# Kernel tuning notes

Measured on AMD Instinct MI355X. Metric: run time of the kernel, lower is better.

The kernel has to match this reference:

```python
import jax, jax.numpy as jnp
import numpy as np

VOCAB, EMBED, HIDDEN, NCLS = 50257, 1024, 4096, 3
B, S = 4096, 128


def ternary_quant(w):
    # Per-tensor ternary quantization: scale = mean |w|, weights in {-s, 0, +s}.
    s = jnp.mean(jnp.abs(w))
    return jnp.round(jnp.clip(w / s, -1.0, 1.0)) * s


def layer_norm(x, g, b, eps=1e-5):
    mu = jnp.mean(x, axis=-1, keepdims=True)
    var = jnp.mean(jnp.square(x - mu), axis=-1, keepdims=True)
    return (x - mu) * jax.lax.rsqrt(var + eps) * g + b


def setup_inputs() -> dict:
    key = jax.random.key(0)
    ks = jax.random.split(key, 12)
    input_ids = jax.random.randint(ks[0], (B, S), 0, VOCAB, dtype=jnp.int32)
    emb = jax.random.normal(ks[1], (VOCAB, EMBED), dtype=jnp.float32) * 0.02
    emb = emb.at[0].set(0.0)  # padding_idx=0
    w1 = jax.random.normal(ks[2], (HIDDEN, EMBED), dtype=jnp.float32) * 0.02
    b1 = jnp.zeros((HIDDEN,), jnp.float32)
    w2 = jax.random.normal(ks[3], (HIDDEN // 2, HIDDEN), dtype=jnp.float32) * 0.02
    b2 = jnp.zeros((HIDDEN // 2,), jnp.float32)
    w3 = jax.random.normal(ks[4], (NCLS, HIDDEN // 2), dtype=jnp.float32) * 0.02
    b3 = jnp.zeros((NCLS,), jnp.float32)
    g1 = jnp.ones((HIDDEN,), jnp.float32)
    beta1 = jnp.zeros((HIDDEN,), jnp.float32)
    g2 = jnp.ones((HIDDEN // 2,), jnp.float32)
    beta2 = jnp.zeros((HIDDEN // 2,), jnp.float32)
    return dict(input_ids=input_ids, emb=emb, w1=w1, b1=b1, w2=w2, b2=b2,
                w3=w3, b3=b3, g1=g1, beta1=beta1, g2=g2, beta2=beta2)


def reference(input_ids, emb, w1, b1, w2, b2, w3, b3, g1, beta1, g2, beta2):
    x = emb[input_ids]                                   # (B, S, E)
    mask = (input_ids != 0).astype(x.dtype)[..., None]   # (B, S, 1)
    x = jnp.sum(x * mask, axis=1) / jnp.clip(jnp.sum(mask, axis=1), 1.0)  # (B, E)
    h = jax.nn.gelu(layer_norm(x @ ternary_quant(w1).T + b1, g1, beta1), approximate=False)
    h = jax.nn.gelu(layer_norm(h @ ternary_quant(w2).T + b2, g2, beta2), approximate=False)
    logits = h @ ternary_quant(w3).T + b3                # (B, 3)
    return logits
```

## Files before the change

kernel.cpp:

```cpp
#include <hip/hip_runtime.h>
#include <cstdint>
#include <cstddef>


#define GAS __attribute__((address_space(1)))
#define LAS __attribute__((address_space(3)))

typedef __bf16 bf16x8 __attribute__((ext_vector_type(8)));
typedef float  f32x4  __attribute__((ext_vector_type(4)));
typedef unsigned short u16x8 __attribute__((ext_vector_type(8)));

__device__ __forceinline__ unsigned short f2bf(float f) {
    unsigned int u = __float_as_uint(f);
    u += 0x7FFFu + ((u >> 16) & 1u);
    return (unsigned short)(u >> 16);
}
__device__ __forceinline__ float bf2f(unsigned short h) {
    return __uint_as_float(((unsigned int)h) << 16);
}

static constexpr int BB = 4096;
static constexpr int SS = 128;
static constexpr int EE = 1024;
static constexpr int HH = 4096;
static constexpr int H2D = 2048;
static constexpr int VOCAB = 50257;

static constexpr size_t MiB      = 1024 * 1024;
static constexpr size_t OFF_S    = 0;
static constexpr size_t OFF_X    = 65536;
static constexpr size_t OFF_EMBH = OFF_X + (size_t)BB * EE * 2;
static constexpr size_t SZ_EMBH  = (size_t)VOCAB * EE * 2;
static constexpr size_t OFF_Q1   = OFF_EMBH;
static constexpr size_t OFF_Q2   = OFF_EMBH + 8 * MiB;
static constexpr size_t OFF_C1   = OFF_EMBH + 24 * MiB;
static constexpr size_t OFF_C2   = OFF_EMBH + 24 * MiB;
static constexpr size_t OFF_H2   = OFF_EMBH;
static constexpr size_t OFF_H1   = OFF_EMBH + SZ_EMBH;


__global__ __launch_bounds__(256) void prep2_kernel(const float* __restrict__ e,
                                                    unsigned short* __restrict__ o,
                                                    const float* __restrict__ w1,
                                                    const float* __restrict__ w2,
                                                    double* __restrict__ part1,
                                                    double* __restrict__ part2) {
    const int bid = blockIdx.x;
    const int tid = threadIdx.x;
    const int n8 = (VOCAB * EE) / 8;
    for (int i = bid * 256 + tid; i < n8; i += 2048 * 256) {
        const float4 v0 = ((const float4*)e)[2 * i];
        const float4 v1 = ((const float4*)e)[2 * i + 1];
        union { unsigned short u[8]; uint4 q; } r;
        r.u[0] = f2bf(v0.x); r.u[1] = f2bf(v0.y); r.u[2] = f2bf(v0.z); r.u[3] = f2bf(v0.w);
        r.u[4] = f2bf(v1.x); r.u[5] = f2bf(v1.y); r.u[6] = f2bf(v1.z); r.u[7] = f2bf(v1.w);
        ((uint4*)o)[i] = r.q;
    }
    const int lane = tid & 63, wid = tid >> 6;
    double a1 = 0.0, a2 = 0.0;
    const int n41 = HH * EE / 4;
    for (int i = bid * 256 + tid; i < n41; i += 2048 * 256) {
        const float4 v = ((const float4*)w1)[i];
        a1 += (double)fabsf(v.x) + (double)fabsf(v.y) + (double)fabsf(v.z) + (double)fabsf(v.w);
    }
    const int n42 = H2D * HH / 4;
    for (int i = bid * 256 + tid; i < n42; i += 2048 * 256) {
        const float4 v = ((const float4*)w2)[i];
        a2 += (double)fabsf(v.x) + (double)fabsf(v.y) + (double)fabsf(v.z) + (double)fabsf(v.w);
    }
    for (int off = 32; off; off >>= 1) { a1 += __shfl_down(a1, off); a2 += __shfl_down(a2, off); }
    __shared__ double r1[4], r2[4];
    if (lane == 0) { r1[wid] = a1; r2[wid] = a2; }
    __syncthreads();
    if (tid == 0) {
        part1[bid] = r1[0] + r1[1] + r1[2] + r1[3];
        part2[bid] = r2[0] + r2[1] + r2[2] + r2[3];
    }
}

__global__ __launch_bounds__(256) void reduce_sums(const double* __restrict__ part1,
                                                   const double* __restrict__ part2,
                                                   const float* __restrict__ w3,
                                                   double* __restrict__ sums) {
    const int bid = blockIdx.x, tid = threadIdx.x;
    const int lane = tid & 63, wid = tid >> 6;
    double acc = 0.0;
    if (bid == 0) {
        for (int i = tid; i < 2048; i += 256) acc += part1[i];
    } else if (bid == 1) {
        for (int i = tid; i < 2048; i += 256) acc += part2[i];
    } else {
        for (int i = tid; i < 3 * H2D; i += 256) acc += (double)fabsf(w3[i]);
    }
    for (int o = 32; o; o >>= 1) acc += __shfl_down(acc, o);
    __shared__ double r[4];
    if (lane == 0) r[wid] = acc;
    __syncthreads();
    if (tid == 0) sums[bid] = r[0] + r[1] + r[2] + r[3];
}

__global__ __launch_bounds__(256) void quant_all(const float* __restrict__ w1,
                                                 const float* __restrict__ w2,
                                                 const double* __restrict__ sums,
                                                 unsigned short* __restrict__ q1,
                                                 unsigned short* __restrict__ q2) {
    const int bid = blockIdx.x;
    const float* w; int n8; unsigned short* q; int b0; int nb; double ssum; double dn;
    if (bid < 2048) { w = w1; n8 = HH * EE / 8;  q = q1; b0 = bid;        nb = 2048; ssum = sums[0]; dn = (double)HH * EE;  }
    else            { w = w2; n8 = H2D * HH / 8; q = q2; b0 = bid - 2048; nb = 4096; ssum = sums[1]; dn = (double)H2D * HH; }
    const float inv_s = (float)(dn / ssum);
    for (int i = b0 * 256 + threadIdx.x; i < n8; i += nb * 256) {
        const float4 v0 = ((const float4*)w)[2 * i];
        const float4 v1 = ((const float4*)w)[2 * i + 1];
        union { unsigned short u[8]; uint4 p; } r;
        const float a[8] = {v0.x, v0.y, v0.z, v0.w, v1.x, v1.y, v1.z, v1.w};
        #pragma unroll
        for (int j = 0; j < 8; ++j)
            r.u[j] = f2bf(rintf(fminf(1.f, fmaxf(-1.f, a[j] * inv_s))));
        ((uint4*)q)[i] = r.p;
    }
}

__global__ __launch_bounds__(256) void pool_kernel(const int* __restrict__ ids,
                                                   const unsigned short* __restrict__ embh,
                                                   unsigned short* __restrict__ X) {
    const int tid = threadIdx.x;
    const int row = tid >> 7;
    const int t   = tid & 127;
    __shared__ int sid[256];
    __shared__ int sorted_ids[2][128];
    __shared__ int cnt[2][64];
    __shared__ int pos[2][64];
    __shared__ int nz[2];
    sid[tid] = ids[(size_t)blockIdx.x * 256 + tid];
    if (tid < 128) ((int*)cnt)[tid] = 0;
    if (tid < 2) nz[tid] = 0;
    __syncthreads();
    const int myid = sid[tid];
    const int ph = myid >> 10;
    atomicAdd(&cnt[row][ph], 1);
    if (myid != 0) atomicAdd(&nz[row], 1);
    __syncthreads();
    if (tid < 2) {
        int s = 0;
        #pragma unroll
        for (int p = 0; p < 64; ++p) { pos[tid][p] = s; s += cnt[tid][p]; }
    }
    __syncthreads();
    const int where = atomicAdd(&pos[row][ph], 1);
    sorted_ids[row][where] = myid;
    __syncthreads();

    const int col = t * 8;
    float a[8] = {};
    #pragma unroll 8
    for (int s = 0; s < 128; ++s) {
        const int id = sorted_ids[row][s];
        const u16x8 v = *(const u16x8*)(embh + (size_t)id * EE + col);
        #pragma unroll
        for (int j = 0; j < 8; ++j) a[j] += bf2f(v[j]);
    }
    const int c = nz[row];
    const float inv = 1.f / (float)(c ? c : 1);
    u16x8 ov;
    #pragma unroll
    for (int j = 0; j < 8; ++j) ov[j] = f2bf(a[j] * inv);
    const int b = blockIdx.x * 2 + row;
    *(u16x8*)(X + (size_t)b * EE + col) = ov;
}


#define FENCE_ asm volatile("" ::: "memory")
#define SBAR_  do { FENCE_; __builtin_amdgcn_s_barrier(); FENCE_; } while (0)
#define WAITLGKM_ do { asm volatile("s_waitcnt lgkmcnt(0)" ::: "memory"); __builtin_amdgcn_sched_barrier(0); } while (0)

#define LDA_(dst, b, i, ks) dst = *(const LAS bf16x8*)((LAS char*)lds + (b) * 32768 + aBase0 + (ks) * 8192 + (i) * 1024)
#define LDB_(dst, b, j, ks) dst = *(const LAS bf16x8*)((LAS char*)lds + (b) * 32768 + bBase0 + (ks) * 8192 + (j) * 1024)

#define STAGE_(gptr, rowBase, t_, slotOff)                                                         \
    {                                                                                              \
        const unsigned short* g0_ = (gptr) + (size_t)((rowBase) + srow) * K + kStart + (t_) * 64 + scol; \
        __builtin_amdgcn_global_load_lds((const GAS void*)g0_,                                     \
            (LAS void*)((LAS char*)lds + (slotOff) + wid * 1024), 16, 0, 0);                       \
        __builtin_amdgcn_global_load_lds((const GAS void*)(g0_ + 32),                              \
            (LAS void*)((LAS char*)lds + (slotOff) + 8192 + wid * 1024), 16, 0, 0);                \
    }

#define MFMA16_(ib, bfA, jb)                                                                       \
    _Pragma("unroll") for (int ii = 0; ii < 4; ++ii) {                                             \
        _Pragma("unroll") for (int jj = 0; jj < 2; ++jj) {                                         \
            f32x4 c_ = acc[(ib) * 4 + ii][(jb) + jj];                                              \
            c_ = __builtin_amdgcn_mfma_f32_16x16x32_bf16(af[ii][0], bfA[jj][0], c_, 0, 0, 0);      \
            c_ = __builtin_amdgcn_mfma_f32_16x16x32_bf16(af[ii][1], bfA[jj][1], c_, 0, 0, 0);      \
            acc[(ib) * 4 + ii][(jb) + jj] = c_;                                                    \
        }                                                                                          \
    }

#define GROUP_(b, t_)                                                                              \
    {                                                                                              \
        _Pragma("unroll") for (int ii = 0; ii < 4; ++ii) { LDA_(af[ii][0], b, ii, 0); LDA_(af[ii][1], b, ii, 1); } \
        _Pragma("unroll") for (int jj = 0; jj < 2; ++jj) { LDB_(bf0[jj][0], b, jj, 0); LDB_(bf0[jj][1], b, jj, 1); } \
        if ((t_) + 1 < NTI) {                                                                      \
            STAGE_(A, mBase, (t_) + 1, ((b) ^ 1) * 32768);                                         \
            STAGE_(A, mBase + 128, (t_) + 1, ((b) ^ 1) * 32768 + 16384);                           \
        }                                                                                          \
        SBAR_; WAITLGKM_;                                                                          \
        __builtin_amdgcn_s_setprio(1); MFMA16_(0, bf0, 0); __builtin_amdgcn_s_setprio(0);          \
        SBAR_;                                                                                     \
        _Pragma("unroll") for (int jj = 0; jj < 2; ++jj) { LDB_(bf1[jj][0], b, 2 + jj, 0); LDB_(bf1[jj][1], b, 2 + jj, 1); } \
        if ((t_) + 1 < NTI) { STAGE_(B, nBase + 128, (t_) + 1, 65536 + ((b) ^ 1) * 32768 + 16384); } \
        SBAR_; WAITLGKM_;                                                                          \
        __builtin_amdgcn_s_setprio(1); MFMA16_(0, bf1, 2); __builtin_amdgcn_s_setprio(0);          \
        SBAR_;                                                                                     \
        _Pragma("unroll") for (int ii = 0; ii < 4; ++ii) { LDA_(af[ii][0], b, 4 + ii, 0); LDA_(af[ii][1], b, 4 + ii, 1); } \
        if ((t_) + 2 < NTI) { STAGE_(B, nBase, (t_) + 2, 65536 + (b) * 32768); }                   \
        SBAR_; WAITLGKM_;                                                                          \
        __builtin_amdgcn_s_setprio(1); MFMA16_(1, bf0, 0); __builtin_amdgcn_s_setprio(0);          \
        SBAR_;                                                                                     \
        __builtin_amdgcn_s_setprio(1); MFMA16_(1, bf1, 2); __builtin_amdgcn_s_setprio(0);          \
        if ((t_) + 2 < NTI) { asm volatile("s_waitcnt vmcnt(2)" ::: "memory"); }                   \
        else               { asm volatile("s_waitcnt vmcnt(0)" ::: "memory"); }                    \
        SBAR_;                                                                                     \
    }

#define GEMM256_CORE(NT_VAL)                                                                       \
    extern __shared__ char lds[];                                                                  \
    constexpr int NTI = (NT_VAL);                                                                  \
    const int tid  = threadIdx.x;                                                                  \
    const int wid  = tid >> 6;                                                                     \
    const int lane = tid & 63;                                                                     \
    const int wm = wid >> 2, wn = wid & 3;                                                         \
    const int quad = lane >> 4;                                                                    \
    const int l16  = lane & 15;                                                                    \
    const int mBase = blockIdx.y * 256;                                                            \
    const int nBase = blockIdx.x * 256;                                                            \
    const int kStart = blockIdx.z * NTI * 64;                                                      \
                    \
                    \
    const int dp   = wid * 1024 + lane * 16;                                                       \
    const int srow = dp >> 6;                                                                      \
    const int sb   = dp & 63;                                                                      \
    const int scol = ((((sb >> 5) & 1) ^ ((srow >> 3) & 1)) << 4) + (((sb >> 4) & 1) << 3);        \
                           \
    const int qoff = ((quad ^ (((l16 >> 3) & 1) << 1)) << 4);                                      \
    const int aBase0 = (wm << 14) + (l16 << 6) + qoff;                                             \
    const int bBase0 = 65536 + ((wn >> 1) << 14) + ((((wn & 1) << 6) + l16) << 6) + qoff;          \
    f32x4 acc[8][4] = {};                                                                          \
    bf16x8 af[4][2], bf0[2][2], bf1[2][2];                                                         \
              \
    STAGE_(A, mBase, 0, 0);                                                                        \
    STAGE_(A, mBase + 128, 0, 16384);                                                              \
    STAGE_(B, nBase, 0, 65536);                                                                    \
    STAGE_(B, nBase + 128, 0, 65536 + 16384);                                                      \
    STAGE_(B, nBase, 1, 65536 + 32768);                                                            \
    asm volatile("s_waitcnt vmcnt(2)" ::: "memory");                                               \
    SBAR_;                                                                                         \
    _Pragma("unroll 1")                                                                            \
    for (int t = 0; t < NTI; t += 2) {                                                             \
        GROUP_(0, t)                                                                               \
        GROUP_(1, t + 1)                                                                           \
    }

__global__ __launch_bounds__(512, 2) void gemm256_c16(const unsigned short* __restrict__ A,
                                                      const unsigned short* __restrict__ B,
                                                      unsigned short* __restrict__ C,
                                                      int M, int N, int K) {
    GEMM256_CORE(16)
    #pragma unroll
    for (int i = 0; i < 8; ++i) {
        const int row0 = mBase + wm * 128 + i * 16 + quad * 4;
        #pragma unroll
        for (int j = 0; j < 4; ++j) {
            const int col = nBase + wn * 64 + j * 16 + l16;
            #pragma unroll
            for (int r = 0; r < 4; ++r)
                C[(size_t)(row0 + r) * N + col] = f2bf(acc[i][j][r]);
        }
    }
}

__global__ __launch_bounds__(512, 2) void gemm256_sk2(const unsigned short* __restrict__ A,
                                                      const unsigned short* __restrict__ B,
                                                      float* __restrict__ Cp,
                                                      int M, int N, int K) {
    GEMM256_CORE(32)
    float* C = Cp + (size_t)blockIdx.z * M * N;
    #pragma unroll
    for (int i = 0; i < 8; ++i) {
        const int row0 = mBase + wm * 128 + i * 16 + quad * 4;
        #pragma unroll
        for (int j = 0; j < 4; ++j) {
            const int col = nBase + wn * 64 + j * 16 + l16;
            #pragma unroll
            for (int r = 0; r < 4; ++r)
                C[(size_t)(row0 + r) * N + col] = acc[i][j][r];
        }
    }
}

__global__ __launch_bounds__(256) void ln_gelu_c16(const unsigned short* __restrict__ Cm,
                                                   const double* __restrict__ ssum, double nw,
                                                   const float* __restrict__ bias,
                                                   const float* __restrict__ gamma,
                                                   const float* __restrict__ beta,
                                                   unsigned short* __restrict__ H, int N) {
    __shared__ float buf[4096];
    __shared__ float redS[4], redQ[4];
    const int row = blockIdx.x, tid = threadIdx.x;
    const int lane = tid & 63, wid = tid >> 6;
    const float s = (float)(ssum[0] / nw);
    float ps = 0.f, pq = 0.f;
    for (int c = tid; c < N; c += 256) {
        const float y = bf2f(Cm[(size_t)row * N + c]) * s + bias[c];
        buf[c] = y;
        ps += y; pq += y * y;
    }
    for (int o = 32; o; o >>= 1) { ps += __shfl_down(ps, o); pq += __shfl_down(pq, o); }
    if (lane == 0) { redS[wid] = ps; redQ[wid] = pq; }
    __syncthreads();
    const float sum = redS[0] + redS[1] + redS[2] + redS[3];
    const float sq  = redQ[0] + redQ[1] + redQ[2] + redQ[3];
    const float mu  = sum / (float)N;
    float var = sq / (float)N - mu * mu;
    var = fmaxf(var, 0.f);
    const float inv = rsqrtf(var + 1e-5f);
    for (int c = tid; c < N; c += 256) {
        const float y = (buf[c] - mu) * inv * gamma[c] + beta[c];
        const float g = 0.5f * y * (1.f + erff(y * 0.70710678118654752f));
        H[(size_t)row * N + c] = f2bf(g);
    }
}

__global__ __launch_bounds__(256) void ln_gelu_2buf(const float* __restrict__ Ca,
                                                    const float* __restrict__ Cb,
                                                    const double* __restrict__ ssum, double nw,
                                                    const float* __restrict__ bias,
                                                    const float* __restrict__ gamma,
                                                    const float* __restrict__ beta,
                                                    unsigned short* __restrict__ H, int N) {
    __shared__ float buf[2048];
    __shared__ float redS[4], redQ[4];
    const int row = blockIdx.x, tid = threadIdx.x;
    const int lane = tid & 63, wid = tid >> 6;
    const float s = (float)(ssum[0] / nw);
    float ps = 0.f, pq = 0.f;
    for (int c = tid; c < N; c += 256) {
        const size_t idx = (size_t)row * N + c;
        const float y = (Ca[idx] + Cb[idx]) * s + bias[c];
        buf[c] = y;
        ps += y; pq += y * y;
    }
    for (int o = 32; o; o >>= 1) { ps += __shfl_down(ps, o); pq += __shfl_down(pq, o); }
    if (lane == 0) { redS[wid] = ps; redQ[wid] = pq; }
    __syncthreads();
    const float sum = redS[0] + redS[1] + redS[2] + redS[3];
    const float sq  = redQ[0] + redQ[1] + redQ[2] + redQ[3];
    const float mu  = sum / (float)N;
    float var = sq / (float)N - mu * mu;
    var = fmaxf(var, 0.f);
    const float inv = rsqrtf(var + 1e-5f);
    for (int c = tid; c < N; c += 256) {
        const float y = (buf[c] - mu) * inv * gamma[c] + beta[c];
        const float g = 0.5f * y * (1.f + erff(y * 0.70710678118654752f));
        H[(size_t)row * N + c] = f2bf(g);
    }
}

__global__ __launch_bounds__(256) void final_kernel(const unsigned short* __restrict__ H2,
                                                    const float* __restrict__ w3,
                                                    const double* __restrict__ ssum,
                                                    const float* __restrict__ b3,
                                                    float* __restrict__ out) {
    const int row = blockIdx.x, tid = threadIdx.x;
    const int lane = tid & 63, wid = tid >> 6;
    const float inv_s3 = (float)((double)(3 * H2D) / ssum[0]);
    float a0 = 0.f, a1 = 0.f, a2 = 0.f;
    for (int k = tid; k < H2D; k += 256) {
        const float h = bf2f(H2[(size_t)row * H2D + k]);
        const float q0 = rintf(fminf(1.f, fmaxf(-1.f, w3[k] * inv_s3)));
        const float q1 = rintf(fminf(1.f, fmaxf(-1.f, w3[H2D + k] * inv_s3)));
        const float q2 = rintf(fminf(1.f, fmaxf(-1.f, w3[2 * H2D + k] * inv_s3)));
        a0 += h * q0; a1 += h * q1; a2 += h * q2;
    }
    for (int o = 32; o; o >>= 1) {
        a0 += __shfl_down(a0, o); a1 += __shfl_down(a1, o); a2 += __shfl_down(a2, o);
    }
    __shared__ float r[3][4];
    if (lane == 0) { r[0][wid] = a0; r[1][wid] = a1; r[2][wid] = a2; }
    __syncthreads();
    if (tid < 3) {
        const float s3 = (float)(ssum[0] / (double)(3 * H2D));
        out[(size_t)row * 3 + tid] =
            (r[tid][0] + r[tid][1] + r[tid][2] + r[tid][3]) * s3 + b3[tid];
    }
}


extern "C" void kernel_launch(void* const* d_in, const int* in_sizes, int n_in,
                              void* d_out, int out_size, void* d_ws, size_t ws_size,
                              hipStream_t stream) {
    const int*   ids = (const int*)d_in[0];
    const float* emb = (const float*)d_in[1];
    const float* w1  = (const float*)d_in[2];
    const float* b1  = (const float*)d_in[3];
    const float* w2  = (const float*)d_in[4];
    const float* b2  = (const float*)d_in[5];
    const float* w3  = (const float*)d_in[6];
    const float* b3  = (const float*)d_in[7];
    const float* g1  = (const float*)d_in[8];
    const float* be1 = (const float*)d_in[9];
    const float* g2  = (const float*)d_in[10];
    const float* be2 = (const float*)d_in[11];
    float* out = (float*)d_out;
    char* ws = (char*)d_ws;

    double*         sums  = (double*)(ws + OFF_S);
    double*         part1 = sums + 8;
    double*         part2 = part1 + 2048;
    unsigned short* X     = (unsigned short*)(ws + OFF_X);
    unsigned short* embh  = (unsigned short*)(ws + OFF_EMBH);
    unsigned short* q1    = (unsigned short*)(ws + OFF_Q1);
    unsigned short* q2    = (unsigned short*)(ws + OFF_Q2);
    unsigned short* C1    = (unsigned short*)(ws + OFF_C1);
    float*          Cp    = (float*)(ws + OFF_C2);
    unsigned short* H1    = (unsigned short*)(ws + OFF_H1);
    unsigned short* H2    = (unsigned short*)(ws + OFF_H2);

    static int gemmAttrDone = 0;
    if (!gemmAttrDone) {
        hipFuncSetAttribute((const void*)gemm256_c16,
                            hipFuncAttributeMaxDynamicSharedMemorySize, 131072);
        hipFuncSetAttribute((const void*)gemm256_sk2,
                            hipFuncAttributeMaxDynamicSharedMemorySize, 131072);
        gemmAttrDone = 1;
    }

    prep2_kernel<<<2048, 256, 0, stream>>>(emb, embh, w1, w2, part1, part2);
    reduce_sums<<<3, 256, 0, stream>>>(part1, part2, w3, sums);
    pool_kernel<<<BB / 2, 256, 0, stream>>>(ids, embh, X);

    quant_all<<<6144, 256, 0, stream>>>(w1, w2, sums, q1, q2);

    gemm256_c16<<<dim3(HH / 256, BB / 256), 512, 131072, stream>>>(X, q1, C1, BB, HH, EE);
    ln_gelu_c16<<<BB, 256, 0, stream>>>(C1, sums + 0, (double)HH * (double)EE,
                                        b1, g1, be1, H1, HH);
    gemm256_sk2<<<dim3(H2D / 256, BB / 256, 2), 512, 131072, stream>>>(H1, q2, Cp, BB, H2D, HH);
    ln_gelu_2buf<<<BB, 256, 0, stream>>>(Cp, Cp + (size_t)BB * H2D, sums + 1,
                                         (double)H2D * (double)HH, b2, g2, be2, H2, H2D);
    final_kernel<<<BB, 256, 0, stream>>>(H2, w3, sums + 2, b3, out);
}
```

Before: 659.1 us.

## Fuse quantization into pooling, LN2+GELU into final classifier, register-resident layer norm

Merges the weight ternary quantization into the pooling kernel, so each pool block also quantizes a slice of w1 and w2. The q1/q2 buffers move to offsets past H1 so they no longer alias the bf16 embedding copy that pooling reads. The second layer-norm+GELU is fused with the 3-class projection, removing the H2 round trip and one launch. Both layer norms now keep values in registers with vectorized loads instead of a shared-memory buffer. This cuts launches and intermediate traffic but adds register pressure and longer pool blocks.

```diff
diff --git a/kernel.cpp b/kernel.cpp
--- a/kernel.cpp
+++ b/kernel.cpp
@@ -31,12 +31,11 @@
 static constexpr size_t OFF_X    = 65536;
 static constexpr size_t OFF_EMBH = OFF_X + (size_t)BB * EE * 2;
 static constexpr size_t SZ_EMBH  = (size_t)VOCAB * EE * 2;
-static constexpr size_t OFF_Q1   = OFF_EMBH;
-static constexpr size_t OFF_Q2   = OFF_EMBH + 8 * MiB;
 static constexpr size_t OFF_C1   = OFF_EMBH + 24 * MiB;
 static constexpr size_t OFF_C2   = OFF_EMBH + 24 * MiB;
-static constexpr size_t OFF_H2   = OFF_EMBH;
 static constexpr size_t OFF_H1   = OFF_EMBH + SZ_EMBH;
+static constexpr size_t OFF_Q1   = OFF_H1 + 32 * MiB;
+static constexpr size_t OFF_Q2   = OFF_Q1 + 8 * MiB;
 
 
 __global__ __launch_bounds__(256) void prep2_kernel(const float* __restrict__ e,
@@ -99,32 +98,17 @@
     if (tid == 0) sums[bid] = r[0] + r[1] + r[2] + r[3];
 }
 
-__global__ __launch_bounds__(256) void quant_all(const float* __restrict__ w1,
-                                                 const float* __restrict__ w2,
-                                                 const double* __restrict__ sums,
-                                                 unsigned short* __restrict__ q1,
-                                                 unsigned short* __restrict__ q2) {
+__global__ __launch_bounds__(256) void pool_quant(const int* __restrict__ ids,
+                                                  const unsigned short* __restrict__ embh,
+                                                  unsigned short* __restrict__ X,
+                                                  const float* __restrict__ w1,
+                                                  const float* __restrict__ w2,
+                                                  const double* __restrict__ sums,
+                                                  unsigned short* __restrict__ q1,
+                                                  unsigned short* __restrict__ q2) {
+    const int tid = threadIdx.x;
     const int bid = blockIdx.x;
-    const float* w; int n8; unsigned short* q; int b0; int nb; double ssum; double dn;
-    if (bid < 2048) { w = w1; n8 = HH * EE / 8;  q = q1; b0 = bid;        nb = 2048; ssum = sums[0]; dn = (double)HH * EE;  }
-    else            { w = w2; n8 = H2D * HH / 8; q = q2; b0 = bid - 2048; nb = 4096; ssum = sums[1]; dn = (double)H2D * HH; }
-    const float inv_s = (float)(dn / ssum);
-    for (int i = b0 * 256 + threadIdx.x; i < n8; i += nb * 256) {
-        const float4 v0 = ((const float4*)w)[2 * i];
-        const float4 v1 = ((const float4*)w)[2 * i + 1];
-        union { unsigned short u[8]; uint4 p; } r;
-        const float a[8] = {v0.x, v0.y, v0.z, v0.w, v1.x, v1.y, v1.z, v1.w};
-        #pragma unroll
-        for (int j = 0; j < 8; ++j)
-            r.u[j] = f2bf(rintf(fminf(1.f, fmaxf(-1.f, a[j] * inv_s))));
-        ((uint4*)q)[i] = r.p;
-    }
-}
-
-__global__ __launch_bounds__(256) void pool_kernel(const int* __restrict__ ids,
-                                                   const unsigned short* __restrict__ embh,
-                                                   unsigned short* __restrict__ X) {
-    const int tid = threadIdx.x;
+
     const int row = tid >> 7;
     const int t   = tid & 127;
     __shared__ int sid[256];
@@ -132,7 +116,7 @@
     __shared__ int cnt[2][64];
     __shared__ int pos[2][64];
     __shared__ int nz[2];
-    sid[tid] = ids[(size_t)blockIdx.x * 256 + tid];
+    sid[tid] = ids[(size_t)bid * 256 + tid];
     if (tid < 128) ((int*)cnt)[tid] = 0;
     if (tid < 2) nz[tid] = 0;
     __syncthreads();
@@ -150,6 +134,34 @@
     const int where = atomicAdd(&pos[row][ph], 1);
     sorted_ids[row][where] = myid;
     __syncthreads();
+
+    {
+        const int i = bid * 256 + tid;
+        const float inv1 = (float)((double)HH * (double)EE / sums[0]);
+        {
+            const float4 v0 = ((const float4*)w1)[2 * i];
+            const float4 v1 = ((const float4*)w1)[2 * i + 1];
+            union { unsigned short u[8]; uint4 p; } r;
+            const float a[8] = {v0.x, v0.y, v0.z, v0.w, v1.x, v1.y, v1.z, v1.w};
+            #pragma unroll
+            for (int j = 0; j < 8; ++j)
+                r.u[j] = f2bf(rintf(fminf(1.f, fmaxf(-1.f, a[j] * inv1))));
+            ((uint4*)q1)[i] = r.p;
+        }
+        const float inv2 = (float)((double)H2D * (double)HH / sums[1]);
+        #pragma unroll
+        for (int k = 0; k < 2; ++k) {
+            const int j8 = i + k * (2048 * 256);
+            const float4 v0 = ((const float4*)w2)[2 * j8];
+            const float4 v1 = ((const float4*)w2)[2 * j8 + 1];
+            union { unsigned short u[8]; uint4 p; } r;
+            const float a[8] = {v0.x, v0.y, v0.z, v0.w, v1.x, v1.y, v1.z, v1.w};
+            #pragma unroll
+            for (int j = 0; j < 8; ++j)
+                r.u[j] = f2bf(rintf(fminf(1.f, fmaxf(-1.f, a[j] * inv2))));
+            ((uint4*)q2)[j8] = r.p;
+        }
+    }
 
     const int col = t * 8;
     float a[8] = {};
@@ -165,7 +177,7 @@
     u16x8 ov;
     #pragma unroll
     for (int j = 0; j < 8; ++j) ov[j] = f2bf(a[j] * inv);
-    const int b = blockIdx.x * 2 + row;
+    const int b = bid * 2 + row;
     *(u16x8*)(X + (size_t)b * EE + col) = ov;
 }
 
@@ -235,19 +247,15 @@
     const int mBase = blockIdx.y * 256;                                                            \
     const int nBase = blockIdx.x * 256;                                                            \
     const int kStart = blockIdx.z * NTI * 64;                                                      \
-                    \
-                    \
     const int dp   = wid * 1024 + lane * 16;                                                       \
     const int srow = dp >> 6;                                                                      \
     const int sb   = dp & 63;                                                                      \
     const int scol = ((((sb >> 5) & 1) ^ ((srow >> 3) & 1)) << 4) + (((sb >> 4) & 1) << 3);        \
-                           \
     const int qoff = ((quad ^ (((l16 >> 3) & 1) << 1)) << 4);                                      \
     const int aBase0 = (wm << 14) + (l16 << 6) + qoff;                                             \
     const int bBase0 = 65536 + ((wn >> 1) << 14) + ((((wn & 1) << 6) + l16) << 6) + qoff;          \
     f32x4 acc[8][4] = {};                                                                          \
     bf16x8 af[4][2], bf0[2][2], bf1[2][2];                                                         \
-              \
     STAGE_(A, mBase, 0, 0);                                                                        \
     STAGE_(A, mBase + 128, 0, 16384);                                                              \
     STAGE_(B, nBase, 0, 65536);                                                                    \
@@ -304,16 +312,25 @@
                                                    const float* __restrict__ gamma,
                                                    const float* __restrict__ beta,
                                                    unsigned short* __restrict__ H, int N) {
-    __shared__ float buf[4096];
     __shared__ float redS[4], redQ[4];
     const int row = blockIdx.x, tid = threadIdx.x;
     const int lane = tid & 63, wid = tid >> 6;
     const float s = (float)(ssum[0] / nw);
+    float y[16];
     float ps = 0.f, pq = 0.f;
-    for (int c = tid; c < N; c += 256) {
-        const float y = bf2f(Cm[(size_t)row * N + c]) * s + bias[c];
-        buf[c] = y;
-        ps += y; pq += y * y;
+    #pragma unroll
+    for (int h = 0; h < 2; ++h) {
+        const int c = h * 2048 + tid * 8;
+        const u16x8 v = *(const u16x8*)(Cm + (size_t)row * N + c);
+        const float4 b0 = *(const float4*)(bias + c);
+        const float4 b1 = *(const float4*)(bias + c + 4);
+        #pragma unroll
+        for (int j = 0; j < 4; ++j) {
+            const float y0 = bf2f(v[j]) * s + ((const float*)&b0)[j];
+            const float y1 = bf2f(v[4 + j]) * s + ((const float*)&b1)[j];
+            y[h * 8 + j] = y0; y[h * 8 + 4 + j] = y1;
+            ps += y0 + y1; pq += y0 * y0 + y1 * y1;
+        }
     }
     for (int o = 32; o; o >>= 1) { ps += __shfl_down(ps, o); pq += __shfl_down(pq, o); }
     if (lane == 0) { redS[wid] = ps; redQ[wid] = pq; }
@@ -324,74 +341,93 @@
     float var = sq / (float)N - mu * mu;
     var = fmaxf(var, 0.f);
     const float inv = rsqrtf(var + 1e-5f);
-    for (int c = tid; c < N; c += 256) {
-        const float y = (buf[c] - mu) * inv * gamma[c] + beta[c];
-        const float g = 0.5f * y * (1.f + erff(y * 0.70710678118654752f));
-        H[(size_t)row * N + c] = f2bf(g);
-    }
-}
-
-__global__ __launch_bounds__(256) void ln_gelu_2buf(const float* __restrict__ Ca,
-                                                    const float* __restrict__ Cb,
-                                                    const double* __restrict__ ssum, double nw,
-                                                    const float* __restrict__ bias,
-                                                    const float* __restrict__ gamma,
-                                                    const float* __restrict__ beta,
-                                                    unsigned short* __restrict__ H, int N) {
-    __shared__ float buf[2048];
+    #pragma unroll
+    for (int h = 0; h < 2; ++h) {
+        const int c = h * 2048 + tid * 8;
+        const float4 g0 = *(const float4*)(gamma + c);
+        const float4 g1 = *(const float4*)(gamma + c + 4);
+        const float4 e0 = *(const float4*)(beta + c);
+        const float4 e1 = *(const float4*)(beta + c + 4);
+        u16x8 ov;
+        #pragma unroll
+        for (int j = 0; j < 4; ++j) {
+            const float z0 = (y[h * 8 + j] - mu) * inv * ((const float*)&g0)[j] + ((const float*)&e0)[j];
+            const float z1 = (y[h * 8 + 4 + j] - mu) * inv * ((const float*)&g1)[j] + ((const float*)&e1)[j];
+            ov[j]     = f2bf(0.5f * z0 * (1.f + erff(z0 * 0.70710678118654752f)));
+            ov[4 + j] = f2bf(0.5f * z1 * (1.f + erff(z1 * 0.70710678118654752f)));
+        }
+        *(u16x8*)(H + (size_t)row * N + c) = ov;
+    }
+}
+
+__global__ __launch_bounds__(256) void ln2_final(const float* __restrict__ Ca,
+                                                 const float* __restrict__ Cb,
+                                                 const double* __restrict__ sums,
+                                                 const float* __restrict__ bias,
+                                                 const float* __restrict__ gamma,
+                                                 const float* __restrict__ beta,
+                                                 const float* __restrict__ w3,
+                                                 const float* __restrict__ b3,
+                                                 float* __restrict__ out) {
     __shared__ float redS[4], redQ[4];
+    __shared__ float rr[3][4];
     const int row = blockIdx.x, tid = threadIdx.x;
     const int lane = tid & 63, wid = tid >> 6;
-    const float s = (float)(ssum[0] / nw);
+    const float s = (float)(sums[1] / ((double)H2D * (double)HH));
+    const int c = tid * 8;
+    const size_t base = (size_t)row * H2D + c;
+    float y[8];
     float ps = 0.f, pq = 0.f;
-    for (int c = tid; c < N; c += 256) {
-        const size_t idx = (size_t)row * N + c;
-        const float y = (Ca[idx] + Cb[idx]) * s + bias[c];
-        buf[c] = y;
-        ps += y; pq += y * y;
+    #pragma unroll
+    for (int h = 0; h < 2; ++h) {
+        const float4 a4 = *(const float4*)(Ca + base + h * 4);
+        const float4 b4 = *(const float4*)(Cb + base + h * 4);
+        const float4 bi = *(const float4*)(bias + c + h * 4);
+        #pragma unroll
+        for (int j = 0; j < 4; ++j) {
+            const float yy = (((const float*)&a4)[j] + ((const float*)&b4)[j]) * s
+                           + ((const float*)&bi)[j];
+            y[h * 4 + j] = yy;
+            ps += yy; pq += yy * yy;
+        }
     }
     for (int o = 32; o; o >>= 1) { ps += __shfl_down(ps, o); pq += __shfl_down(pq, o); }
     if (lane == 0) { redS[wid] = ps; redQ[wid] = pq; }
     __syncthreads();
     const float sum = redS[0] + redS[1] + redS[2] + redS[3];
     const float sq  = redQ[0] + redQ[1] + redQ[2] + redQ[3];
-    const float mu  = sum / (float)N;
-    float var = sq / (float)N - mu * mu;
+    const float mu  = sum / (float)H2D;
+    float var = sq / (float)H2D - mu * mu;
     var = fmaxf(var, 0.f);
     const float inv = rsqrtf(var + 1e-5f);
-    for (int c = tid; c < N; c += 256) {
-        const float y = (buf[c] - mu) * inv * gamma[c] + beta[c];
-        const float g = 0.5f * y * (1.f + erff(y * 0.70710678118654752f));
-        H[(size_t)row * N + c] = f2bf(g);
-    }
-}
-
-__global__ __launch_bounds__(256) void final_kernel(const unsigned short* __restrict__ H2,
-                                                    const float* __restrict__ w3,
-                                                    const double* __restrict__ ssum,
-                                                    const float* __restrict__ b3,
-                                                    float* __restrict__ out) {
-    const int row = blockIdx.x, tid = threadIdx.x;
-    const int lane = tid & 63, wid = tid >> 6;
-    const float inv_s3 = (float)((double)(3 * H2D) / ssum[0]);
+    const float inv_s3 = (float)((double)(3 * H2D) / sums[2]);
     float a0 = 0.f, a1 = 0.f, a2 = 0.f;
-    for (int k = tid; k < H2D; k += 256) {
-        const float h = bf2f(H2[(size_t)row * H2D + k]);
-        const float q0 = rintf(fminf(1.f, fmaxf(-1.f, w3[k] * inv_s3)));
-        const float q1 = rintf(fminf(1.f, fmaxf(-1.f, w3[H2D + k] * inv_s3)));
-        const float q2 = rintf(fminf(1.f, fmaxf(-1.f, w3[2 * H2D + k] * inv_s3)));
-        a0 += h * q0; a1 += h * q1; a2 += h * q2;
+    #pragma unroll
+    for (int h = 0; h < 2; ++h) {
+        const float4 g4 = *(const float4*)(gamma + c + h * 4);
+        const float4 e4 = *(const float4*)(beta + c + h * 4);
+        const float4 w0 = *(const float4*)(w3 + c + h * 4);
+        const float4 w1_ = *(const float4*)(w3 + H2D + c + h * 4);
+        const float4 w2_ = *(const float4*)(w3 + 2 * H2D + c + h * 4);
+        #pragma unroll
+        for (int j = 0; j < 4; ++j) {
+            const float z = (y[h * 4 + j] - mu) * inv * ((const float*)&g4)[j]
+                          + ((const float*)&e4)[j];
+            const float g = 0.5f * z * (1.f + erff(z * 0.70710678118654752f));
+            a0 += g * rintf(fminf(1.f, fmaxf(-1.f, ((const float*)&w0)[j]  * inv_s3)));
+            a1 += g * rintf(fminf(1.f, fmaxf(-1.f, ((const float*)&w1_)[j] * inv_s3)));
+            a2 += g * rintf(fminf(1.f, fmaxf(-1.f, ((const float*)&w2_)[j] * inv_s3)));
+        }
     }
     for (int o = 32; o; o >>= 1) {
         a0 += __shfl_down(a0, o); a1 += __shfl_down(a1, o); a2 += __shfl_down(a2, o);
     }
-    __shared__ float r[3][4];
-    if (lane == 0) { r[0][wid] = a0; r[1][wid] = a1; r[2][wid] = a2; }
+    if (lane == 0) { rr[0][wid] = a0; rr[1][wid] = a1; rr[2][wid] = a2; }
     __syncthreads();
     if (tid < 3) {
-        const float s3 = (float)(ssum[0] / (double)(3 * H2D));
+        const float s3 = (float)(sums[2] / (double)(3 * H2D));
         out[(size_t)row * 3 + tid] =
-            (r[tid][0] + r[tid][1] + r[tid][2] + r[tid][3]) * s3 + b3[tid];
+            (rr[tid][0] + rr[tid][1] + rr[tid][2] + rr[tid][3]) * s3 + b3[tid];
     }
 }
 
@@ -424,7 +460,6 @@
     unsigned short* C1    = (unsigned short*)(ws + OFF_C1);
     float*          Cp    = (float*)(ws + OFF_C2);
     unsigned short* H1    = (unsigned short*)(ws + OFF_H1);
-    unsigned short* H2    = (unsigned short*)(ws + OFF_H2);
 
     static int gemmAttrDone = 0;
     if (!gemmAttrDone) {
@@ -437,15 +472,13 @@
 
     prep2_kernel<<<2048, 256, 0, stream>>>(emb, embh, w1, w2, part1, part2);
     reduce_sums<<<3, 256, 0, stream>>>(part1, part2, w3, sums);
-    pool_kernel<<<BB / 2, 256, 0, stream>>>(ids, embh, X);
-
-    quant_all<<<6144, 256, 0, stream>>>(w1, w2, sums, q1, q2);
+
+    pool_quant<<<BB / 2, 256, 0, stream>>>(ids, embh, X, w1, w2, sums, q1, q2);
 
     gemm256_c16<<<dim3(HH / 256, BB / 256), 512, 131072, stream>>>(X, q1, C1, BB, HH, EE);
     ln_gelu_c16<<<BB, 256, 0, stream>>>(C1, sums + 0, (double)HH * (double)EE,
                                         b1, g1, be1, H1, HH);
     gemm256_sk2<<<dim3(H2D / 256, BB / 256, 2), 512, 131072, stream>>>(H1, q2, Cp, BB, H2D, HH);
-    ln_gelu_2buf<<<BB, 256, 0, stream>>>(Cp, Cp + (size_t)BB * H2D, sums + 1,
-                                         (double)H2D * (double)HH, b2, g2, be2, H2, H2D);
-    final_kernel<<<BB, 256, 0, stream>>>(H2, w3, sums + 2, b3, out);
-}
+    ln2_final<<<BB, 256, 0, stream>>>(Cp, Cp + (size_t)BB * H2D, sums,
+                                      b2, g2, be2, w3, b3, out);
+}
```

Result: faster. 626.0 us (-5.0%).
